# Kernel optimization log

Measured on AMD Instinct MI355X. Metric: run time of the kernel, lower is better.

The kernel has to match this reference:

```python
import jax, jax.numpy as jnp
import numpy as np

N_NODES = 100000
N_EDGES = 3200000
F_IN = 128
NOUT = 32


def _lin(x, W, b):
    return x @ W + b


def _spect_conv(x, src, dst, W, b, n_nodes):
    # edge_attr is all-ones with a single frequency (K=1), so SpectConv reduces to
    # an unweighted scatter-add of linearly transformed source-node features.
    h = x @ W                                   # [N, nout]
    agg = jax.ops.segment_sum(h[src], dst, num_segments=n_nodes)  # [N, nout]
    return agg + b


def setup_inputs() -> dict:
    key = jax.random.key(0)
    ks = jax.random.split(key, 32)
    s = 0.05

    def w(k, shape):
        return jax.random.normal(k, shape, dtype=jnp.float32) * s

    inp = {
        "x": jax.random.normal(ks[0], (N_NODES, F_IN), dtype=jnp.float32),
        "edge_index": jax.random.randint(ks[1], (2, N_EDGES), 0, N_NODES, dtype=jnp.int32),
        # SpectConv weights (single frequency) + biases
        "Wc1": w(ks[2], (F_IN, NOUT)), "bc1": jnp.zeros((NOUT,), jnp.float32),
        "Wc2": w(ks[3], (NOUT, NOUT)), "bc2": jnp.zeros((NOUT,), jnp.float32),
        "Wc3": w(ks[4], (NOUT, NOUT)), "bc3": jnp.zeros((NOUT,), jnp.float32),
        # dense branch weights
        "W11": w(ks[5], (F_IN, NOUT)), "b11": w(ks[6], (NOUT,)),
        "W12": w(ks[7], (F_IN, NOUT)), "b12": w(ks[8], (NOUT,)),
        "W13": w(ks[9], (F_IN, NOUT)), "b13": w(ks[10], (NOUT,)),
        "W21": w(ks[11], (NOUT, NOUT)), "b21": w(ks[12], (NOUT,)),
        "W22": w(ks[13], (NOUT, NOUT)), "b22": w(ks[14], (NOUT,)),
        "W23": w(ks[15], (NOUT, NOUT)), "b23": w(ks[16], (NOUT,)),
        "W31": w(ks[17], (NOUT, NOUT)), "b31": w(ks[18], (NOUT,)),
        "W32": w(ks[19], (NOUT, NOUT)), "b32": w(ks[20], (NOUT,)),
        "W33": w(ks[21], (NOUT, NOUT)), "b33": w(ks[22], (NOUT,)),
        "W2": w(ks[23], (NOUT, 1)), "b2": w(ks[24], (1,)),
    }
    return inp


def reference(x, edge_index,
              Wc1, bc1, Wc2, bc2, Wc3, bc3,
              W11, b11, W12, b12, W13, b13,
              W21, b21, W22, b22, W23, b23,
              W31, b31, W32, b32, W33, b33,
              W2, b2):
    src, dst = edge_index[0], edge_index[1]
    n = x.shape[0]
    relu = jax.nn.relu

    def block(h, Wa, ba, Wc, bc, Wm1, bm1, Wm2, bm2):
        return (relu(_lin(h, Wa, ba))
                + relu(_spect_conv(h, src, dst, Wc, bc, n))
                + relu(_lin(h, Wm1, bm1) * _lin(h, Wm2, bm2)))

    h = block(x, W11, b11, Wc1, bc1, W12, b12, W13, b13)
    h = block(h, W21, b21, Wc2, bc2, W22, b22, W23, b23)
    h = block(h, W31, b31, Wc3, bc3, W32, b32, W33, b33)
    return _lin(h, W2, b2)
```

## Files before the change

kernel.cpp:

```cpp
#include <hip/hip_runtime.h>
#include <hip/hip_bf16.h>

#define N_FEAT 32
#define CBITS 7
#define CAP   6000
#define CTILE 4096

typedef __attribute__((ext_vector_type(8))) short short8;
typedef __attribute__((ext_vector_type(4))) float floatx4;

static __device__ __forceinline__ unsigned short f2b(float f) {
    unsigned u = __float_as_uint(f);
    return (unsigned short)((u + 0x7FFFu + ((u >> 16) & 1u)) >> 16);
}
static __device__ __forceinline__ float b2f(unsigned short b) {
    return __uint_as_float(((unsigned)b) << 16);
}

struct CoarseS {
    unsigned sorted[CTILE];
    unsigned hist[1024];
    unsigned lbase[1024];
    unsigned gofs[1024];
    unsigned part[512];
};
union FatS {
    unsigned short sW[128][136];
    CoarseS s;
};

__global__ __launch_bounds__(512)
void fused_transform_sort_kernel(const float* __restrict__ x,
                                 const float* __restrict__ Wa, const float* __restrict__ ba,
                                 const float* __restrict__ Wc,
                                 const float* __restrict__ Wm1, const float* __restrict__ bm1,
                                 const float* __restrict__ Wm2, const float* __restrict__ bm2,
                                 unsigned short* __restrict__ t_pre,
                                 unsigned short* __restrict__ t_c,
                                 int n_nodes, int tf_grid,
                                 const int* __restrict__ src, const int* __restrict__ dst,
                                 unsigned* __restrict__ cnt_g, unsigned* __restrict__ binned,
                                 int n_edges, int n_buckets)
{
    __shared__ FatS u;
    const int t = threadIdx.x;

    if ((int)blockIdx.x < tf_grid) {
        constexpr int K = 128;
        const int node0 = blockIdx.x * 128;
        const int wave = t >> 6;
        const int lane = t & 63;
        const int m16 = lane & 15;
        const int quad = lane >> 4;

        for (int i = t; i < 128 * K; i += 512) {
            const int c = i & 127, kk = i >> 7;
            const int mat = c >> 5, cl = c & 31;
            const float* W = (mat == 0) ? Wa : (mat == 1) ? Wc : (mat == 2) ? Wm1 : Wm2;
            u.sW[c][kk] = f2b(W[(size_t)kk * 32 + cl]);
        }
        __syncthreads();

        const int n = node0 + wave * 16 + m16;
        const bool nok = (n < n_nodes);

        floatx4 acc[8];
#pragma unroll
        for (int i = 0; i < 8; ++i) acc[i] = (floatx4){0.f, 0.f, 0.f, 0.f};

#pragma unroll
        for (int k0 = 0; k0 < K; k0 += 32) {
            short8 a;
            if (nok) {
                const float4 v0 = *reinterpret_cast<const float4*>(x + (size_t)n * K + k0 + quad * 8);
                const float4 v1 = *reinterpret_cast<const float4*>(x + (size_t)n * K + k0 + quad * 8 + 4);
                union { short8 v; unsigned short uu[8]; } pk;
                pk.uu[0] = f2b(v0.x); pk.uu[1] = f2b(v0.y); pk.uu[2] = f2b(v0.z); pk.uu[3] = f2b(v0.w);
                pk.uu[4] = f2b(v1.x); pk.uu[5] = f2b(v1.y); pk.uu[6] = f2b(v1.z); pk.uu[7] = f2b(v1.w);
                a = pk.v;
            } else {
                a = (short8){0,0,0,0,0,0,0,0};
            }
#pragma unroll
            for (int t8 = 0; t8 < 8; ++t8) {
                const short8 b = *reinterpret_cast<const short8*>(&u.sW[t8 * 16 + m16][k0 + quad * 8]);
                acc[t8] = __builtin_amdgcn_mfma_f32_16x16x32_bf16(a, b, acc[t8], 0, 0, 0);
            }
        }

#pragma unroll
        for (int r = 0; r < 4; ++r) {
            const int node = node0 + wave * 16 + quad * 4 + r;
            if (node < n_nodes) {
#pragma unroll
                for (int half = 0; half < 2; ++half) {
                    const int c = m16 + half * 16;
                    const float av  = acc[0 + half][r] + ba[c];
                    const float wcv = acc[2 + half][r];
                    const float m1  = acc[4 + half][r] + bm1[c];
                    const float m2  = acc[6 + half][r] + bm2[c];
                    t_pre[(size_t)node * N_FEAT + c] = f2b(fmaxf(av, 0.f) + fmaxf(m1 * m2, 0.f));
                    t_c[(size_t)node * N_FEAT + c] = f2b(wcv);
                }
            }
        }
    } else {
        CoarseS& s = u.s;
        const int blk = blockIdx.x - tf_grid;
        const int e0 = blk * CTILE;
        const int cnt = min(CTILE, n_edges - e0);
        if (cnt <= 0) return;

        for (int i = t; i < 1024; i += 512) s.hist[i] = 0;
        __syncthreads();
        for (int i = t; i < cnt; i += 512)
            atomicAdd(&s.hist[(unsigned)dst[e0 + i] >> CBITS], 1u);
        __syncthreads();

        const unsigned c0 = s.hist[2 * t], c1 = s.hist[2 * t + 1];
        s.part[t] = c0 + c1;
        __syncthreads();
        for (int off = 1; off < 512; off <<= 1) {
            const unsigned v = (t >= off) ? s.part[t - off] : 0u;
            __syncthreads();
            s.part[t] += v;
            __syncthreads();
        }
        const unsigned base = (t == 0) ? 0u : s.part[t - 1];
        s.lbase[2 * t] = base;
        s.lbase[2 * t + 1] = base + c0;

        for (int i = t; i < n_buckets; i += 512) {
            const unsigned h = s.hist[i];
            s.gofs[i] = h ? atomicAdd(&cnt_g[i], h) : 0u;
        }
        for (int i = t; i < 1024; i += 512) s.hist[i] = 0;
        __syncthreads();

        for (int i = t; i < cnt; i += 512) {
            const unsigned d = (unsigned)dst[e0 + i];
            const unsigned sv = (unsigned)src[e0 + i];
            const unsigned b = d >> CBITS;
            const unsigned pos = s.lbase[b] + atomicAdd(&s.hist[b], 1u);
            s.sorted[pos] = ((d & ((1u << CBITS) - 1)) << 17) | sv;
        }
        __syncthreads();

        for (int i = t; i < n_buckets; i += 512) {
            const unsigned lb = s.lbase[i], n = s.hist[i], g0 = s.gofs[i];
            for (unsigned j = 0; j < n; ++j) {
                const unsigned gp = g0 + j;
                if (gp < CAP) binned[(size_t)i * CAP + gp] = s.sorted[lb + j];
            }
        }
    }
}

__global__ __launch_bounds__(256)
void transform32_kernel(const unsigned short* __restrict__ hin,
                        const float* __restrict__ Wa, const float* __restrict__ ba,
                        const float* __restrict__ Wc,
                        const float* __restrict__ Wm1, const float* __restrict__ bm1,
                        const float* __restrict__ Wm2, const float* __restrict__ bm2,
                        unsigned short* __restrict__ t_pre, unsigned short* __restrict__ t_c,
                        int n_nodes)
{
    constexpr int K = 32;
    __shared__ unsigned short sW[128][40];

    const int t = threadIdx.x;
    const int node0 = blockIdx.x * 64;
    const int wave = t >> 6;
    const int lane = t & 63;
    const int m16 = lane & 15;
    const int quad = lane >> 4;

    for (int i = t; i < 128 * K; i += 256) {
        const int c = i & 127, kk = i >> 7;
        const int mat = c >> 5, cl = c & 31;
        const float* W = (mat == 0) ? Wa : (mat == 1) ? Wc : (mat == 2) ? Wm1 : Wm2;
        sW[c][kk] = f2b(W[(size_t)kk * 32 + cl]);
    }
    __syncthreads();

    const int n = node0 + wave * 16 + m16;
    const bool nok = (n < n_nodes);

    floatx4 acc[8];
#pragma unroll
    for (int i = 0; i < 8; ++i) acc[i] = (floatx4){0.f, 0.f, 0.f, 0.f};

    const short8 a = nok ? *reinterpret_cast<const short8*>(hin + (size_t)n * K + quad * 8)
                         : (short8){0,0,0,0,0,0,0,0};
#pragma unroll
    for (int t8 = 0; t8 < 8; ++t8) {
        const short8 b = *reinterpret_cast<const short8*>(&sW[t8 * 16 + m16][quad * 8]);
        acc[t8] = __builtin_amdgcn_mfma_f32_16x16x32_bf16(a, b, acc[t8], 0, 0, 0);
    }

#pragma unroll
    for (int r = 0; r < 4; ++r) {
        const int node = node0 + wave * 16 + quad * 4 + r;
        if (node < n_nodes) {
#pragma unroll
            for (int half = 0; half < 2; ++half) {
                const int c = m16 + half * 16;
                const float av  = acc[0 + half][r] + ba[c];
                const float wcv = acc[2 + half][r];
                const float m1  = acc[4 + half][r] + bm1[c];
                const float m2  = acc[6 + half][r] + bm2[c];
                t_pre[(size_t)node * N_FEAT + c] = f2b(fmaxf(av, 0.f) + fmaxf(m1 * m2, 0.f));
                t_c[(size_t)node * N_FEAT + c] = f2b(wcv);
            }
        }
    }
}

__global__ __launch_bounds__(512)
void fine_sort_kernel(const unsigned* __restrict__ binned,
                      const unsigned* __restrict__ cnt_g,
                      unsigned* __restrict__ total_ctr,
                      int* __restrict__ srcs,
                      unsigned* __restrict__ rowstart, unsigned* __restrict__ rowend,
                      int n_nodes, int n_buckets)
{
    __shared__ int sorted_src[CAP];
    __shared__ unsigned hist[512];
    __shared__ unsigned incl[512];
    __shared__ unsigned ebase[512];
    __shared__ unsigned ob_s;

    const int t = threadIdx.x;
    const int b = blockIdx.x;
    const unsigned cnt = min(cnt_g[b], (unsigned)CAP);
    const int node0 = b << CBITS;
    const int nodes_here = min(128, n_nodes - node0);
    const unsigned* tile = binned + (size_t)b * CAP;

    if (t == 0) ob_s = atomicAdd(total_ctr, cnt);
    hist[t] = 0;
    __syncthreads();
    const unsigned ob = ob_s;

    for (unsigned i = t; i < cnt; i += 512) {
        const unsigned e = tile[i];
        atomicAdd(&hist[((e >> 17) << 2) | ((e & 0x1FFFFu) >> 15)], 1u);
    }
    __syncthreads();

    const unsigned myh = hist[t];
    incl[t] = myh;
    __syncthreads();
    for (int off = 1; off < 512; off <<= 1) {
        const unsigned v = (t >= off) ? incl[t - off] : 0u;
        __syncthreads();
        incl[t] += v;
        __syncthreads();
    }
    ebase[t] = incl[t] - myh;
    __syncthreads();

    if (t < nodes_here) {
        rowstart[node0 + t] = ob + ebase[t << 2];
        rowend[node0 + t]   = ob + incl[(t << 2) + 3];
    }

    hist[t] = 0;
    __syncthreads();
    for (unsigned i = t; i < cnt; i += 512) {
        const unsigned e = tile[i];
        const unsigned key = ((e >> 17) << 2) | ((e & 0x1FFFFu) >> 15);
        const unsigned pos = ebase[key] + atomicAdd(&hist[key], 1u);
        sorted_src[pos] = (int)(e & 0x1FFFFu);
    }
    __syncthreads();
    for (unsigned i = t; i < cnt; i += 512)
        srcs[ob + i] = sorted_src[i];
}

static __device__ __forceinline__ void add8(float* a, short8 v) {
#pragma unroll
    for (int j = 0; j < 8; ++j) a[j] += b2f((unsigned short)v[j]);
}

__global__ __launch_bounds__(256)
void gather_combine_kernel(const unsigned short* __restrict__ t_c,
                           const unsigned short* __restrict__ t_pre,
                           const unsigned* __restrict__ rowstart,
                           const unsigned* __restrict__ rowend,
                           const int* __restrict__ srcs,
                           const float* __restrict__ bc, unsigned short* __restrict__ hout,
                           int n_nodes)
{
    const int node = blockIdx.x * 64 + (threadIdx.x >> 2);
    const int l4 = threadIdx.x & 3;
    const int f0 = l4 * 8;
    if (node >= n_nodes) return;
    const unsigned lo = rowstart[node], hi = rowend[node];
    float acc[8] = {0.f, 0.f, 0.f, 0.f, 0.f, 0.f, 0.f, 0.f};
    unsigned i = lo;
    for (; i + 8 <= hi; i += 8) {
        short8 v[8];
#pragma unroll
        for (int j = 0; j < 8; ++j)
            v[j] = *reinterpret_cast<const short8*>(t_c + (size_t)srcs[i + j] * N_FEAT + f0);
#pragma unroll
        for (int j = 0; j < 8; ++j) add8(acc, v[j]);
    }
    for (; i + 4 <= hi; i += 4) {
        short8 v[4];
#pragma unroll
        for (int j = 0; j < 4; ++j)
            v[j] = *reinterpret_cast<const short8*>(t_c + (size_t)srcs[i + j] * N_FEAT + f0);
#pragma unroll
        for (int j = 0; j < 4; ++j) add8(acc, v[j]);
    }
    for (; i < hi; ++i)
        add8(acc, *reinterpret_cast<const short8*>(t_c + (size_t)srcs[i] * N_FEAT + f0));

    const short8 p = *reinterpret_cast<const short8*>(t_pre + (size_t)node * N_FEAT + f0);
    union { short8 v; unsigned short u[8]; } r;
#pragma unroll
    for (int j = 0; j < 8; ++j)
        r.u[j] = f2b(b2f((unsigned short)p[j]) + fmaxf(acc[j] + bc[f0 + j], 0.f));
    *reinterpret_cast<short8*>(hout + (size_t)node * N_FEAT + f0) = r.v;
}

__global__ __launch_bounds__(256)
void gather_final_kernel(const unsigned short* __restrict__ t_c,
                         const unsigned short* __restrict__ t_pre,
                         const unsigned* __restrict__ rowstart,
                         const unsigned* __restrict__ rowend,
                         const int* __restrict__ srcs,
                         const float* __restrict__ bc, const float* __restrict__ W2,
                         const float* __restrict__ b2, float* __restrict__ out,
                         int n_nodes)
{
    const int node = blockIdx.x * 64 + (threadIdx.x >> 2);
    const int l4 = threadIdx.x & 3;
    const int f0 = l4 * 8;
    if (node >= n_nodes) return;
    const unsigned lo = rowstart[node], hi = rowend[node];
    float acc[8] = {0.f, 0.f, 0.f, 0.f, 0.f, 0.f, 0.f, 0.f};
    unsigned i = lo;
    for (; i + 8 <= hi; i += 8) {
        short8 v[8];
#pragma unroll
        for (int j = 0; j < 8; ++j)
            v[j] = *reinterpret_cast<const short8*>(t_c + (size_t)srcs[i + j] * N_FEAT + f0);
#pragma unroll
        for (int j = 0; j < 8; ++j) add8(acc, v[j]);
    }
    for (; i + 4 <= hi; i += 4) {
        short8 v[4];
#pragma unroll
        for (int j = 0; j < 4; ++j)
            v[j] = *reinterpret_cast<const short8*>(t_c + (size_t)srcs[i + j] * N_FEAT + f0);
#pragma unroll
        for (int j = 0; j < 4; ++j) add8(acc, v[j]);
    }
    for (; i < hi; ++i)
        add8(acc, *reinterpret_cast<const short8*>(t_c + (size_t)srcs[i] * N_FEAT + f0));

    const short8 p = *reinterpret_cast<const short8*>(t_pre + (size_t)node * N_FEAT + f0);
    float r = 0.f;
#pragma unroll
    for (int j = 0; j < 8; ++j)
        r += (b2f((unsigned short)p[j]) + fmaxf(acc[j] + bc[f0 + j], 0.f)) * W2[f0 + j];
    r += __shfl_down(r, 2, 4);
    r += __shfl_down(r, 1, 4);
    if (l4 == 0) out[node] = r + b2[0];
}

extern "C" void kernel_launch(void* const* d_in, const int* in_sizes, int n_in,
                              void* d_out, int out_size, void* d_ws, size_t ws_size,
                              hipStream_t stream)
{
    const float* x   = (const float*)d_in[0];
    const int*   ei  = (const int*)d_in[1];
    const float* Wc1 = (const float*)d_in[2];  const float* bc1 = (const float*)d_in[3];
    const float* Wc2 = (const float*)d_in[4];  const float* bc2 = (const float*)d_in[5];
    const float* Wc3 = (const float*)d_in[6];  const float* bc3 = (const float*)d_in[7];
    const float* W11 = (const float*)d_in[8];  const float* b11 = (const float*)d_in[9];
    const float* W12 = (const float*)d_in[10]; const float* b12 = (const float*)d_in[11];
    const float* W13 = (const float*)d_in[12]; const float* b13 = (const float*)d_in[13];
    const float* W21 = (const float*)d_in[14]; const float* b21 = (const float*)d_in[15];
    const float* W22 = (const float*)d_in[16]; const float* b22 = (const float*)d_in[17];
    const float* W23 = (const float*)d_in[18]; const float* b23 = (const float*)d_in[19];
    const float* W31 = (const float*)d_in[20]; const float* b31 = (const float*)d_in[21];
    const float* W32 = (const float*)d_in[22]; const float* b32 = (const float*)d_in[23];
    const float* W33 = (const float*)d_in[24]; const float* b33 = (const float*)d_in[25];
    const float* W2  = (const float*)d_in[26]; const float* b2  = (const float*)d_in[27];

    const int n_nodes = in_sizes[0] / 128;
    const int n_edges = in_sizes[1] / 2;
    const int* src = ei;
    const int* dst = ei + n_edges;
    const int n_buckets = (n_nodes + (1 << CBITS) - 1) >> CBITS;

    const size_t feat_elems = (size_t)n_nodes * N_FEAT;

    unsigned short* tpre     = (unsigned short*)d_ws;
    unsigned short* tc       = tpre + feat_elems;
    unsigned short* hbuf     = tc + feat_elems;
    int*            srcs     = (int*)(hbuf + feat_elems);
    unsigned*       rowstart = (unsigned*)(srcs + n_edges);
    unsigned*       rowend   = rowstart + n_nodes;
    unsigned*       cnt_g    = rowend + n_nodes;
    unsigned*       binned   = cnt_g + (n_buckets + 1);

    const int tf_grid128 = (n_nodes + 127) / 128;
    const int cb_grid    = (n_edges + CTILE - 1) / CTILE;
    const int tf_grid64  = (n_nodes + 63) / 64;
    const int gc_grid    = (n_nodes + 63) / 64;

    hipMemsetAsync(cnt_g, 0, ((size_t)n_buckets + 1) * sizeof(unsigned), stream);
    fused_transform_sort_kernel<<<tf_grid128 + cb_grid, 512, 0, stream>>>(
        x, W11, b11, Wc1, W12, b12, W13, b13, tpre, tc, n_nodes, tf_grid128,
        src, dst, cnt_g, binned, n_edges, n_buckets);

    fine_sort_kernel<<<n_buckets, 512, 0, stream>>>(
        binned, cnt_g, cnt_g + n_buckets, srcs, rowstart, rowend, n_nodes, n_buckets);

    gather_combine_kernel<<<gc_grid, 256, 0, stream>>>(
        tc, tpre, rowstart, rowend, srcs, bc1, hbuf, n_nodes);

    transform32_kernel<<<tf_grid64, 256, 0, stream>>>(
        hbuf, W21, b21, Wc2, W22, b22, W23, b23, tpre, tc, n_nodes);
    gather_combine_kernel<<<gc_grid, 256, 0, stream>>>(
        tc, tpre, rowstart, rowend, srcs, bc2, hbuf, n_nodes);

    transform32_kernel<<<tf_grid64, 256, 0, stream>>>(
        hbuf, W31, b31, Wc3, W32, b32, W33, b33, tpre, tc, n_nodes);
    gather_final_kernel<<<gc_grid, 256, 0, stream>>>(
        tc, tpre, rowstart, rowend, srcs, bc3, W2, b2, (float*)d_out, n_nodes);
}
```

Before: 348.8 us.

## Split fused transform/sort kernel, widen coarse binning, use wave-shuffle scans

```diff
diff --git a/kernel.cpp b/kernel.cpp
--- a/kernel.cpp
+++ b/kernel.cpp
@@ -4,7 +4,7 @@
 #define N_FEAT 32
 #define CBITS 7
 #define CAP   6000
-#define CTILE 4096
+#define TILE  8192
 
 typedef __attribute__((ext_vector_type(8))) short short8;
 typedef __attribute__((ext_vector_type(4))) float floatx4;
@@ -17,156 +17,18 @@
     return __uint_as_float(((unsigned)b) << 16);
 }
 
-struct CoarseS {
-    unsigned sorted[CTILE];
-    unsigned hist[1024];
-    unsigned lbase[1024];
-    unsigned gofs[1024];
-    unsigned part[512];
-};
-union FatS {
-    unsigned short sW[128][136];
-    CoarseS s;
-};
-
-__global__ __launch_bounds__(512)
-void fused_transform_sort_kernel(const float* __restrict__ x,
-                                 const float* __restrict__ Wa, const float* __restrict__ ba,
-                                 const float* __restrict__ Wc,
-                                 const float* __restrict__ Wm1, const float* __restrict__ bm1,
-                                 const float* __restrict__ Wm2, const float* __restrict__ bm2,
-                                 unsigned short* __restrict__ t_pre,
-                                 unsigned short* __restrict__ t_c,
-                                 int n_nodes, int tf_grid,
-                                 const int* __restrict__ src, const int* __restrict__ dst,
-                                 unsigned* __restrict__ cnt_g, unsigned* __restrict__ binned,
-                                 int n_edges, int n_buckets)
-{
-    __shared__ FatS u;
-    const int t = threadIdx.x;
-
-    if ((int)blockIdx.x < tf_grid) {
-        constexpr int K = 128;
-        const int node0 = blockIdx.x * 128;
-        const int wave = t >> 6;
-        const int lane = t & 63;
-        const int m16 = lane & 15;
-        const int quad = lane >> 4;
-
-        for (int i = t; i < 128 * K; i += 512) {
-            const int c = i & 127, kk = i >> 7;
-            const int mat = c >> 5, cl = c & 31;
-            const float* W = (mat == 0) ? Wa : (mat == 1) ? Wc : (mat == 2) ? Wm1 : Wm2;
-            u.sW[c][kk] = f2b(W[(size_t)kk * 32 + cl]);
-        }
-        __syncthreads();
-
-        const int n = node0 + wave * 16 + m16;
-        const bool nok = (n < n_nodes);
-
-        floatx4 acc[8];
-#pragma unroll
-        for (int i = 0; i < 8; ++i) acc[i] = (floatx4){0.f, 0.f, 0.f, 0.f};
-
-#pragma unroll
-        for (int k0 = 0; k0 < K; k0 += 32) {
-            short8 a;
-            if (nok) {
-                const float4 v0 = *reinterpret_cast<const float4*>(x + (size_t)n * K + k0 + quad * 8);
-                const float4 v1 = *reinterpret_cast<const float4*>(x + (size_t)n * K + k0 + quad * 8 + 4);
-                union { short8 v; unsigned short uu[8]; } pk;
-                pk.uu[0] = f2b(v0.x); pk.uu[1] = f2b(v0.y); pk.uu[2] = f2b(v0.z); pk.uu[3] = f2b(v0.w);
-                pk.uu[4] = f2b(v1.x); pk.uu[5] = f2b(v1.y); pk.uu[6] = f2b(v1.z); pk.uu[7] = f2b(v1.w);
-                a = pk.v;
-            } else {
-                a = (short8){0,0,0,0,0,0,0,0};
-            }
-#pragma unroll
-            for (int t8 = 0; t8 < 8; ++t8) {
-                const short8 b = *reinterpret_cast<const short8*>(&u.sW[t8 * 16 + m16][k0 + quad * 8]);
-                acc[t8] = __builtin_amdgcn_mfma_f32_16x16x32_bf16(a, b, acc[t8], 0, 0, 0);
-            }
-        }
-
-#pragma unroll
-        for (int r = 0; r < 4; ++r) {
-            const int node = node0 + wave * 16 + quad * 4 + r;
-            if (node < n_nodes) {
-#pragma unroll
-                for (int half = 0; half < 2; ++half) {
-                    const int c = m16 + half * 16;
-                    const float av  = acc[0 + half][r] + ba[c];
-                    const float wcv = acc[2 + half][r];
-                    const float m1  = acc[4 + half][r] + bm1[c];
-                    const float m2  = acc[6 + half][r] + bm2[c];
-                    t_pre[(size_t)node * N_FEAT + c] = f2b(fmaxf(av, 0.f) + fmaxf(m1 * m2, 0.f));
-                    t_c[(size_t)node * N_FEAT + c] = f2b(wcv);
-                }
-            }
-        }
-    } else {
-        CoarseS& s = u.s;
-        const int blk = blockIdx.x - tf_grid;
-        const int e0 = blk * CTILE;
-        const int cnt = min(CTILE, n_edges - e0);
-        if (cnt <= 0) return;
-
-        for (int i = t; i < 1024; i += 512) s.hist[i] = 0;
-        __syncthreads();
-        for (int i = t; i < cnt; i += 512)
-            atomicAdd(&s.hist[(unsigned)dst[e0 + i] >> CBITS], 1u);
-        __syncthreads();
-
-        const unsigned c0 = s.hist[2 * t], c1 = s.hist[2 * t + 1];
-        s.part[t] = c0 + c1;
-        __syncthreads();
-        for (int off = 1; off < 512; off <<= 1) {
-            const unsigned v = (t >= off) ? s.part[t - off] : 0u;
-            __syncthreads();
-            s.part[t] += v;
-            __syncthreads();
-        }
-        const unsigned base = (t == 0) ? 0u : s.part[t - 1];
-        s.lbase[2 * t] = base;
-        s.lbase[2 * t + 1] = base + c0;
-
-        for (int i = t; i < n_buckets; i += 512) {
-            const unsigned h = s.hist[i];
-            s.gofs[i] = h ? atomicAdd(&cnt_g[i], h) : 0u;
-        }
-        for (int i = t; i < 1024; i += 512) s.hist[i] = 0;
-        __syncthreads();
-
-        for (int i = t; i < cnt; i += 512) {
-            const unsigned d = (unsigned)dst[e0 + i];
-            const unsigned sv = (unsigned)src[e0 + i];
-            const unsigned b = d >> CBITS;
-            const unsigned pos = s.lbase[b] + atomicAdd(&s.hist[b], 1u);
-            s.sorted[pos] = ((d & ((1u << CBITS) - 1)) << 17) | sv;
-        }
-        __syncthreads();
-
-        for (int i = t; i < n_buckets; i += 512) {
-            const unsigned lb = s.lbase[i], n = s.hist[i], g0 = s.gofs[i];
-            for (unsigned j = 0; j < n; ++j) {
-                const unsigned gp = g0 + j;
-                if (gp < CAP) binned[(size_t)i * CAP + gp] = s.sorted[lb + j];
-            }
-        }
-    }
-}
-
+template <int K, bool BF16_IN>
 __global__ __launch_bounds__(256)
-void transform32_kernel(const unsigned short* __restrict__ hin,
-                        const float* __restrict__ Wa, const float* __restrict__ ba,
-                        const float* __restrict__ Wc,
-                        const float* __restrict__ Wm1, const float* __restrict__ bm1,
-                        const float* __restrict__ Wm2, const float* __restrict__ bm2,
-                        unsigned short* __restrict__ t_pre, unsigned short* __restrict__ t_c,
-                        int n_nodes)
-{
-    constexpr int K = 32;
-    __shared__ unsigned short sW[128][40];
+void transform_mfma_kernel(const void* __restrict__ hin,
+                           const float* __restrict__ Wa, const float* __restrict__ ba,
+                           const float* __restrict__ Wc,
+                           const float* __restrict__ Wm1, const float* __restrict__ bm1,
+                           const float* __restrict__ Wm2, const float* __restrict__ bm2,
+                           unsigned short* __restrict__ t_pre, unsigned short* __restrict__ t_c,
+                           int n_nodes)
+{
+    constexpr int WPITCH = (K == 32) ? 40 : 136;
+    __shared__ unsigned short sW[128][WPITCH];
 
     const int t = threadIdx.x;
     const int node0 = blockIdx.x * 64;
@@ -190,12 +52,31 @@
 #pragma unroll
     for (int i = 0; i < 8; ++i) acc[i] = (floatx4){0.f, 0.f, 0.f, 0.f};
 
-    const short8 a = nok ? *reinterpret_cast<const short8*>(hin + (size_t)n * K + quad * 8)
-                         : (short8){0,0,0,0,0,0,0,0};
-#pragma unroll
-    for (int t8 = 0; t8 < 8; ++t8) {
-        const short8 b = *reinterpret_cast<const short8*>(&sW[t8 * 16 + m16][quad * 8]);
-        acc[t8] = __builtin_amdgcn_mfma_f32_16x16x32_bf16(a, b, acc[t8], 0, 0, 0);
+#pragma unroll
+    for (int k0 = 0; k0 < K; k0 += 32) {
+        short8 a;
+        if (BF16_IN) {
+            const unsigned short* hb = (const unsigned short*)hin;
+            a = nok ? *reinterpret_cast<const short8*>(hb + (size_t)n * K + k0 + quad * 8)
+                    : (short8){0,0,0,0,0,0,0,0};
+        } else {
+            const float* hf = (const float*)hin;
+            if (nok) {
+                const float4 v0 = *reinterpret_cast<const float4*>(hf + (size_t)n * K + k0 + quad * 8);
+                const float4 v1 = *reinterpret_cast<const float4*>(hf + (size_t)n * K + k0 + quad * 8 + 4);
+                union { short8 v; unsigned short u[8]; } pk;
+                pk.u[0] = f2b(v0.x); pk.u[1] = f2b(v0.y); pk.u[2] = f2b(v0.z); pk.u[3] = f2b(v0.w);
+                pk.u[4] = f2b(v1.x); pk.u[5] = f2b(v1.y); pk.u[6] = f2b(v1.z); pk.u[7] = f2b(v1.w);
+                a = pk.v;
+            } else {
+                a = (short8){0,0,0,0,0,0,0,0};
+            }
+        }
+#pragma unroll
+        for (int t8 = 0; t8 < 8; ++t8) {
+            const short8 b = *reinterpret_cast<const short8*>(&sW[t8 * 16 + m16][k0 + quad * 8]);
+            acc[t8] = __builtin_amdgcn_mfma_f32_16x16x32_bf16(a, b, acc[t8], 0, 0, 0);
+        }
     }
 
 #pragma unroll
@@ -216,6 +97,78 @@
     }
 }
 
+__global__ __launch_bounds__(1024)
+void coarse_bin_kernel(const int* __restrict__ src, const int* __restrict__ dst,
+                       unsigned* __restrict__ cnt_g, unsigned* __restrict__ binned,
+                       int n_edges, int n_buckets)
+{
+    __shared__ unsigned sorted[TILE];
+    __shared__ unsigned short buck[TILE];
+    __shared__ unsigned hist[1024];
+    __shared__ unsigned lbase[1024];
+    __shared__ unsigned gofs[1024];
+    __shared__ unsigned wsum[16], woff[16];
+
+    const int t = threadIdx.x;
+    const int wave = t >> 6, lane = t & 63;
+    const int e0 = blockIdx.x * TILE;
+    const int cnt = min(TILE, n_edges - e0);
+    if (cnt <= 0) return;
+
+    hist[t] = 0;
+    __syncthreads();
+
+    unsigned dv[TILE / 1024], sv[TILE / 1024];
+    int nk = 0;
+    for (int i = t; i < cnt; i += 1024, ++nk) {
+        dv[nk] = (unsigned)dst[e0 + i];
+        sv[nk] = (unsigned)src[e0 + i];
+        atomicAdd(&hist[dv[nk] >> CBITS], 1u);
+    }
+    __syncthreads();
+
+    const unsigned myh = hist[t];
+    if (t < n_buckets)
+        gofs[t] = myh ? atomicAdd(&cnt_g[t], myh) : 0u;
+
+    unsigned v = myh;
+#pragma unroll
+    for (int off = 1; off < 64; off <<= 1) {
+        const unsigned nv = __shfl_up(v, off);
+        if (lane >= off) v += nv;
+    }
+    if (lane == 63) wsum[wave] = v;
+    __syncthreads();
+    if (t < 16) {
+        unsigned s = wsum[t];
+#pragma unroll
+        for (int off = 1; off < 16; off <<= 1) {
+            const unsigned nv = __shfl_up(s, off, 16);
+            if (t >= off) s += nv;
+        }
+        woff[t] = s - wsum[t];
+    }
+    hist[t] = 0;
+    __syncthreads();
+    const unsigned lb_mine = v + woff[wave] - myh;
+    lbase[t] = lb_mine;
+    __syncthreads();
+
+    for (int k = 0; k < nk; ++k) {
+        const unsigned b = dv[k] >> CBITS;
+        const unsigned pos = lbase[b] + atomicAdd(&hist[b], 1u);
+        sorted[pos] = ((dv[k] & ((1u << CBITS) - 1)) << 17) | sv[k];
+        buck[pos] = (unsigned short)b;
+    }
+    __syncthreads();
+
+    for (int p = t; p < cnt; p += 1024) {
+        const unsigned b = buck[p];
+        const unsigned gp = gofs[b] + ((unsigned)p - lbase[b]);
+        if (gp < CAP) binned[(size_t)b * CAP + gp] = sorted[p];
+    }
+}
+
 __global__ __launch_bounds__(512)
 void fine_sort_kernel(const unsigned* __restrict__ binned,
                       const unsigned* __restrict__ cnt_g,
@@ -228,9 +181,11 @@
     __shared__ unsigned hist[512];
     __shared__ unsigned incl[512];
     __shared__ unsigned ebase[512];
+    __shared__ unsigned wsum[8], woff[8];
     __shared__ unsigned ob_s;
 
     const int t = threadIdx.x;
+    const int wave = t >> 6, lane = t & 63;
     const int b = blockIdx.x;
     const unsigned cnt = min(cnt_g[b], (unsigned)CAP);
     const int node0 = b << CBITS;
@@ -249,15 +204,28 @@
     __syncthreads();
 
     const unsigned myh = hist[t];
-    incl[t] = myh;
-    __syncthreads();
-    for (int off = 1; off < 512; off <<= 1) {
-        const unsigned v = (t >= off) ? incl[t - off] : 0u;
-        __syncthreads();
-        incl[t] += v;
-        __syncthreads();
-    }
-    ebase[t] = incl[t] - myh;
+    unsigned v = myh;
+#pragma unroll
+    for (int off = 1; off < 64; off <<= 1) {
+        const unsigned nv = __shfl_up(v, off);
+        if (lane >= off) v += nv;
+    }
+    if (lane == 63) wsum[wave] = v;
+    __syncthreads();
+    if (t < 8) {
+        unsigned s = wsum[t];
+#pragma unroll
+        for (int off = 1; off < 8; off <<= 1) {
+            const unsigned nv = __shfl_up(s, off, 8);
+            if (t >= off) s += nv;
+        }
+        woff[t] = s - wsum[t];
+    }
+    hist[t] = 0;
+    __syncthreads();
+    const unsigned my_incl = v + woff[wave];
+    incl[t] = my_incl;
+    ebase[t] = my_incl - myh;
     __syncthreads();
 
     if (t < nodes_here) {
@@ -265,8 +233,6 @@
         rowend[node0 + t]   = ob + incl[(t << 2) + 3];
     }
 
-    hist[t] = 0;
-    __syncthreads();
     for (unsigned i = t; i < cnt; i += 512) {
         const unsigned e = tile[i];
         const unsigned key = ((e >> 17) << 2) | ((e & 0x1FFFFu) >> 15);
@@ -409,28 +375,26 @@
     unsigned*       cnt_g    = rowend + n_nodes;
     unsigned*       binned   = cnt_g + (n_buckets + 1);
 
-    const int tf_grid128 = (n_nodes + 127) / 128;
-    const int cb_grid    = (n_edges + CTILE - 1) / CTILE;
-    const int tf_grid64  = (n_nodes + 63) / 64;
-    const int gc_grid    = (n_nodes + 63) / 64;
+    const int tf_grid = (n_nodes + 63) / 64;
+    const int gc_grid = (n_nodes + 63) / 64;
+    const int cb_grid = (n_edges + TILE - 1) / TILE;
 
     hipMemsetAsync(cnt_g, 0, ((size_t)n_buckets + 1) * sizeof(unsigned), stream);
-    fused_transform_sort_kernel<<<tf_grid128 + cb_grid, 512, 0, stream>>>(
-        x, W11, b11, Wc1, W12, b12, W13, b13, tpre, tc, n_nodes, tf_grid128,
-        src, dst, cnt_g, binned, n_edges, n_buckets);
-
+    coarse_bin_kernel<<<cb_grid, 1024, 0, stream>>>(src, dst, cnt_g, binned, n_edges, n_buckets);
     fine_sort_kernel<<<n_buckets, 512, 0, stream>>>(
         binned, cnt_g, cnt_g + n_buckets, srcs, rowstart, rowend, n_nodes, n_buckets);
 
+    transform_mfma_kernel<128, false><<<tf_grid, 256, 0, stream>>>(
+        x, W11, b11, Wc1, W12, b12, W13, b13, tpre, tc, n_nodes);
     gather_combine_kernel<<<gc_grid, 256, 0, stream>>>(
         tc, tpre, rowstart, rowend, srcs, bc1, hbuf, n_nodes);
 
-    transform32_kernel<<<tf_grid64, 256, 0, stream>>>(
+    transform_mfma_kernel<32, true><<<tf_grid, 256, 0, stream>>>(
         hbuf, W21, b21, Wc2, W22, b22, W23, b23, tpre, tc, n_nodes);
     gather_combine_kernel<<<gc_grid, 256, 0, stream>>>(
         tc, tpre, rowstart, rowend, srcs, bc2, hbuf, n_nodes);
 
-    transform32_kernel<<<tf_grid64, 256, 0, stream>>>(
+    transform_mfma_kernel<32, true><<<tf_grid, 256, 0, stream>>>(
         hbuf, W31, b31, Wc3, W32, b32, W33, b33, tpre, tc, n_nodes);
     gather_final_kernel<<<gc_grid, 256, 0, stream>>>(
         tc, tpre, rowstart, rowend, srcs, bc3, W2, b2, (float*)d_out, n_nodes);
```

New measurement: 342.6 us. Within noise of the previous version (-1.8%).
